# Optimization experiments

Measured on AMD Instinct MI355X. Metric: run time of the kernel, lower is better.

Reference implementation:

```python
import jax, jax.numpy as jnp
import numpy as np

NBITS = 8
NUM_HEADS = 6


def _quant(x, alpha, nbits=NBITS):
    # LSQ-style fake quantization with straight-through estimator.
    qn = -(2 ** (nbits - 1))        # -128
    qp = 2 ** (nbits - 1) - 1       # 127
    s = jnp.clip(x / alpha, qn, qp)
    s = s + jax.lax.stop_gradient(jnp.round(s) - s)  # STE round
    return s * alpha


def setup_inputs() -> dict:
    key = jax.random.key(0)
    ks = jax.random.split(key, 12)
    B, N, C = 2, 2048, 384
    x = jax.random.normal(ks[0], (B, N, C), dtype=jnp.float32)
    w_qkv = jax.random.normal(ks[1], (3 * C, C), dtype=jnp.float32) * 0.02
    w_proj = jax.random.normal(ks[2], (C, C), dtype=jnp.float32) * 0.02
    b_proj = jnp.zeros((C,), dtype=jnp.float32)

    def alpha(k, lo, hi):
        return jax.random.uniform(k, (1,), dtype=jnp.float32, minval=lo, maxval=hi)

    return {
        "x": x,
        "w_qkv": w_qkv,
        "w_proj": w_proj,
        "b_proj": b_proj,
        "a_qkv_w": alpha(ks[3], 0.001, 0.005),
        "a_qkv_a": alpha(ks[4], 0.02, 0.05),
        "a_proj_w": alpha(ks[5], 0.001, 0.005),
        "a_proj_a": alpha(ks[6], 0.02, 0.05),
        "a_q": alpha(ks[7], 0.01, 0.03),
        "a_k": alpha(ks[8], 0.01, 0.03),
        "a_v": alpha(ks[9], 0.01, 0.03),
        "a_attn": alpha(ks[10], 0.01, 0.03),
        "a_attn2": alpha(ks[11], 0.005, 0.01),
    }


def reference(x, w_qkv, w_proj, b_proj, a_qkv_w, a_qkv_a, a_proj_w, a_proj_a,
              a_q, a_k, a_v, a_attn, a_attn2):
    B, N, C = x.shape
    H = NUM_HEADS
    D = C // H
    scale = D ** (-0.5)

    # quantized qkv linear (no bias)
    qkv = _quant(x, a_qkv_a) @ _quant(w_qkv, a_qkv_w).T          # [B,N,3C]
    qkv = qkv.reshape(B, N, 3, H, D).transpose(2, 0, 3, 1, 4)    # [3,B,H,N,D]
    q, k, v = qkv[0], qkv[1], qkv[2]
    q = _quant(q, a_q)
    k = _quant(k, a_k)
    v = _quant(v, a_v)

    attn = jnp.einsum("bhnd,bhmd->bhnm", q, k) * scale           # [B,H,N,N]
    attn = _quant(attn, a_attn)
    attn = jax.nn.softmax(attn, axis=-1)
    attn = _quant(attn, a_attn2)

    out = jnp.einsum("bhnm,bhmd->bhnd", attn, v)                 # [B,H,N,D]
    out = out.transpose(0, 2, 1, 3).reshape(B, N, C)

    # quantized output projection (with bias)
    out = _quant(out, a_proj_a) @ _quant(w_proj, a_proj_w).T + b_proj
    return out
```

## Files before the change

### kernel.cpp

```cpp
#include <hip/hip_runtime.h>
#include <math.h>


typedef int i32x4 __attribute__((ext_vector_type(4)));
typedef float f32x2 __attribute__((ext_vector_type(2)));

#define MFMA_I8(a, b, c) __builtin_amdgcn_mfma_i32_16x16x64_i8(a, b, c, 0, 0, 0)

__device__ __forceinline__ float qclip(float s) {
  return fminf(fmaxf(s, -128.0f), 127.0f);
}

__device__ __forceinline__ float fdivn(float x, float c, float rc) {
  float q0 = x * rc;
  float e = fmaf(-c, q0, x);
  return fmaf(e, rc, q0);
}

__device__ __forceinline__ f32x2 fdivn2(f32x2 x, f32x2 c, f32x2 rc) {
  f32x2 q0 = x * rc;
  f32x2 e = __builtin_elementwise_fma(-c, q0, x);
  return __builtin_elementwise_fma(e, rc, q0);
}

__device__ __forceinline__ void quant16_body(const float* __restrict__ in,
                                             signed char* __restrict__ out,
                                             float a, int i) {
  const float ra = 1.0f / a;
  const float4* p = (const float4*)in + 4 * (size_t)i;
  union { uint4 u; signed char c[16]; } o;
#pragma unroll
  for (int u = 0; u < 4; ++u) {
    float4 v = p[u];
    o.c[4 * u + 0] = (signed char)(int)rintf(qclip(fdivn(v.x, a, ra)));
    o.c[4 * u + 1] = (signed char)(int)rintf(qclip(fdivn(v.y, a, ra)));
    o.c[4 * u + 2] = (signed char)(int)rintf(qclip(fdivn(v.z, a, ra)));
    o.c[4 * u + 3] = (signed char)(int)rintf(qclip(fdivn(v.w, a, ra)));
  }
  *(uint4*)(out + 16 * (size_t)i) = o.u;
}

__global__ __launch_bounds__(256)
void prep(const float* __restrict__ x, const float* __restrict__ wqkv,
          const float* __restrict__ wproj,
          signed char* __restrict__ xq, signed char* __restrict__ wqq,
          signed char* __restrict__ wpq, float* __restrict__ E2,
          const float* __restrict__ a_qkv_a, const float* __restrict__ a_qkv_w,
          const float* __restrict__ a_proj_w, const float* __restrict__ aattn) {
  const int b = blockIdx.x, t = threadIdx.x;
  if (b < 384) {
    int i = b * 256 + t;
    if (i < 98304) quant16_body(x, xq, a_qkv_a[0], i);
  } else if (b < 492) {
    int i = (b - 384) * 256 + t;
    if (i < 27648) quant16_body(wqkv, wqq, a_qkv_w[0], i);
  } else if (b < 528) {
    int i = (b - 492) * 256 + t;
    if (i < 9216) quant16_body(wproj, wpq, a_proj_w[0], i);
  } else {
    int i = (b - 528) * 256 + t;
    float a = aattn[0];
    int vm = (i >> 8) - 128;
    int s = (i & 255) - 128;
    float m = a * (float)vm;
    E2[i] = expf(a * (float)s - m);
  }
}

__global__ __launch_bounds__(256)
void gemm_qkv(const signed char* __restrict__ A, const signed char* __restrict__ W,
              signed char* __restrict__ qws, signed char* __restrict__ kws,
              signed char* __restrict__ vwsT,
              const float* __restrict__ aa, const float* __restrict__ aw,
              const float* __restrict__ aq, const float* __restrict__ ak,
              const float* __restrict__ av) {
  __shared__ int red[2 * 64 * 33];
  const int t = threadIdx.x;
  const int w = t >> 6, lane = t & 63;
  const int lm = lane & 15, quad = lane >> 4;
  const int kw = w >> 1, nw = w & 1;
  const int m0 = blockIdx.x * 64;
  const int n0 = blockIdx.y * 64 + nw * 32;
  i32x4 acc[4][2] = {};
#pragma unroll
  for (int kk = 0; kk < 3; ++kk) {
    int k0 = kw * 192 + kk * 64;
    i32x4 af[4], bf[2];
#pragma unroll
    for (int mt = 0; mt < 4; ++mt)
      af[mt] = *(const i32x4*)(A + (size_t)(m0 + mt * 16 + lm) * 384 + k0 + quad * 16);
#pragma unroll
    for (int nt = 0; nt < 2; ++nt)
      bf[nt] = *(const i32x4*)(W + (size_t)(n0 + nt * 16 + lm) * 384 + k0 + quad * 16);
#pragma unroll
    for (int mt = 0; mt < 4; ++mt)
#pragma unroll
      for (int nt = 0; nt < 2; ++nt)
        acc[mt][nt] = MFMA_I8(af[mt], bf[nt], acc[mt][nt]);
  }
  if (kw == 1) {
    int* rw = red + nw * 2112 + lane * 33;
#pragma unroll
    for (int mt = 0; mt < 4; ++mt)
#pragma unroll
      for (int nt = 0; nt < 2; ++nt)
#pragma unroll
        for (int r = 0; r < 4; ++r)
          rw[mt * 8 + nt * 4 + r] = acc[mt][nt][r];
  }
  __syncthreads();
  if (kw == 0) {
    const int* rw = red + nw * 2112 + lane * 33;
    const float sAB = aa[0] * aw[0];
    const float vaq = aq[0], vak = ak[0], vav = av[0];
    const float rq = 1.0f / vaq, rk = 1.0f / vak, rv = 1.0f / vav;
#pragma unroll
    for (int mt = 0; mt < 4; ++mt) {
#pragma unroll
      for (int nt = 0; nt < 2; ++nt) {
        int cg = n0 + nt * 16 + lm;
        int t3 = cg / 384;
        int rem = cg - t3 * 384;
        int h = rem >> 6, d = rem & 63;
#pragma unroll
        for (int r = 0; r < 4; ++r) {
          int m = m0 + mt * 16 + quad * 4 + r;
          int bb = m >> 11, nn = m & 2047;
          int bh = bb * 6 + h;
          int sum = acc[mt][nt][r] + rw[mt * 8 + nt * 4 + r];
          float val = (float)sum * sAB;
          if (t3 == 0) {
            qws[((size_t)(bh * 2048 + nn) << 6) + d] =
                (signed char)(int)rintf(qclip(fdivn(val, vaq, rq)));
          } else if (t3 == 1) {
            kws[((size_t)(bh * 2048 + nn) << 6) + d] =
                (signed char)(int)rintf(qclip(fdivn(val, vak, rk)));
          } else {
            vwsT[((size_t)((bh << 6) + d) << 11) + nn] =
                (signed char)(int)rintf(qclip(fdivn(val, vav, rv)));
          }
        }
      }
    }
  }
}

#define TROW 2064
__global__ __launch_bounds__(256)
void attn_fused(const signed char* __restrict__ qws, const signed char* __restrict__ kws,
                const signed char* __restrict__ vwsT, const float* __restrict__ E2,
                signed char* __restrict__ ows,
                const float* __restrict__ aq, const float* __restrict__ ak,
                const float* __restrict__ aattn, const float* __restrict__ aattn2,
                const float* __restrict__ av, const float* __restrict__ apa) {
  __shared__ signed char tileS[16 * TROW];
  __shared__ float EfS[4 * 257];
  const int t = threadIdx.x;
  const int w = t >> 6, lane = t & 63;
  const int lm = lane & 15, quad = lane >> 4;
  const int i0 = blockIdx.x * 16;
  const int bh = blockIdx.y;

  const signed char* Qb = qws + ((size_t)bh << 17);
  const signed char* Kb = kws + ((size_t)bh << 17);

  i32x4 bq = *(const i32x4*)(Qb + ((size_t)(i0 + lm) << 6) + quad * 16);
  const float sc = aq[0] * ak[0] * 0.125f;
  const float ia = aattn[0];
  const float ria = 1.0f / ia;
  const f32x2 ia2v = {ia, ia}, ria2v = {ria, ria}, sc2v = {sc, sc};
#pragma unroll 4
  for (int ct = 0; ct < 32; ++ct) {
    int col0 = (w << 9) + ct * 16;
    i32x4 akf = *(const i32x4*)(Kb + ((size_t)(col0 + lm) << 6) + quad * 16);
    i32x4 z = {};
    i32x4 acc = MFMA_I8(akf, bq, z);
    f32x2 sv01 = {(float)acc[0], (float)acc[1]};
    f32x2 sv23 = {(float)acc[2], (float)acc[3]};
    f32x2 q01 = fdivn2(sv01 * sc2v, ia2v, ria2v);
    f32x2 q23 = fdivn2(sv23 * sc2v, ia2v, ria2v);
    union { unsigned int u; signed char c[4]; } pk;
    pk.c[0] = (signed char)(int)rintf(qclip(q01.x));
    pk.c[1] = (signed char)(int)rintf(qclip(q01.y));
    pk.c[2] = (signed char)(int)rintf(qclip(q23.x));
    pk.c[3] = (signed char)(int)rintf(qclip(q23.y));
    *(unsigned int*)(tileS + lm * TROW + col0 + quad * 4) = pk.u;
  }
  __syncthreads();

  const float a2 = aattn2[0];
  const float ra2 = 1.0f / a2;
  const f32x2 a22v = {a2, a2}, ra22v = {ra2, ra2};
  float* Efw = EfS + w * 257;
#pragma unroll
  for (int rr = 0; rr < 4; ++rr) {
    const int row = w * 4 + rr;
    char4* prow = (char4*)(tileS + row * TROW);
    char4 vals[8];
    int vmax = -129;
#pragma unroll
    for (int u = 0; u < 8; ++u) {
      vals[u] = prow[lane + (u << 6)];
      vmax = max(vmax, (int)vals[u].x);
      vmax = max(vmax, (int)vals[u].y);
      vmax = max(vmax, (int)vals[u].z);
      vmax = max(vmax, (int)vals[u].w);
    }
#pragma unroll
    for (int off = 32; off > 0; off >>= 1)
      vmax = max(vmax, __shfl_xor(vmax, off, 64));
#pragma unroll
    for (int u = 0; u < 4; ++u)
      Efw[u * 64 + lane] = E2[((vmax + 128) << 8) + u * 64 + lane];
    const float* Er = Efw + 128;
    float ge[8][4];
    float l = 0.0f;
#pragma unroll
    for (int u = 0; u < 8; ++u) {
      ge[u][0] = Er[(int)vals[u].x];
      ge[u][1] = Er[(int)vals[u].y];
      ge[u][2] = Er[(int)vals[u].z];
      ge[u][3] = Er[(int)vals[u].w];
      l += ge[u][0];
      l += ge[u][1];
      l += ge[u][2];
      l += ge[u][3];
    }
#pragma unroll
    for (int off = 32; off > 0; off >>= 1)
      l += __shfl_xor(l, off, 64);
    const float rl = 1.0f / l;
    const f32x2 l2v = {l, l}, rl2v = {rl, rl};
#pragma unroll
    for (int u = 0; u < 8; ++u) {
      f32x2 g01 = {ge[u][0], ge[u][1]};
      f32x2 g23 = {ge[u][2], ge[u][3]};
      f32x2 t01 = fdivn2(fdivn2(g01, l2v, rl2v), a22v, ra22v);
      f32x2 t23 = fdivn2(fdivn2(g23, l2v, rl2v), a22v, ra22v);
      union { unsigned int ui; signed char c[4]; } pk;
      pk.c[0] = (signed char)(int)rintf(qclip(t01.x));
      pk.c[1] = (signed char)(int)rintf(qclip(t01.y));
      pk.c[2] = (signed char)(int)rintf(qclip(t23.x));
      pk.c[3] = (signed char)(int)rintf(qclip(t23.y));
      *(unsigned int*)(prow + lane + (u << 6)) = pk.ui;
    }
  }
  __syncthreads();

  i32x4 areg[8];
  {
    const signed char* srow = tileS + lm * TROW + (w << 9) + quad * 16;
#pragma unroll
    for (int js = 0; js < 8; ++js)
      areg[js] = *(const i32x4*)(srow + js * 64);
  }
  const signed char* Vb = vwsT + ((size_t)bh << 17) + (w << 9);
  i32x4 acc[4] = {};
#pragma unroll
  for (int js = 0; js < 8; ++js) {
    int j0 = js * 64;
    i32x4 bf[4];
#pragma unroll
    for (int nt = 0; nt < 4; ++nt)
      bf[nt] = *(const i32x4*)(Vb + ((size_t)(nt * 16 + lm) << 11) + j0 + quad * 16);
#pragma unroll
    for (int nt = 0; nt < 4; ++nt)
      acc[nt] = MFMA_I8(areg[js], bf[nt], acc[nt]);
  }

  int* red = (int*)tileS;
  __syncthreads();
  if (w > 0) {
    int* rw = red + (w - 1) * 1088 + lane * 17;
#pragma unroll
    for (int nt = 0; nt < 4; ++nt)
#pragma unroll
      for (int r = 0; r < 4; ++r)
        rw[nt * 4 + r] = acc[nt][r];
  }
  __syncthreads();
  if (w == 0) {
    const float so = a2 * av[0];
    const float ipa = apa[0];
    const float ripa = 1.0f / ipa;
    int bb = bh / 6, h = bh % 6;
#pragma unroll
    for (int nt = 0; nt < 4; ++nt) {
      int d = nt * 16 + lm;
#pragma unroll
      for (int r = 0; r < 4; ++r) {
        int s = acc[nt][r] + red[lane * 17 + nt * 4 + r]
              + red[1088 + lane * 17 + nt * 4 + r]
              + red[2176 + lane * 17 + nt * 4 + r];
        int i = i0 + quad * 4 + r;
        ows[(size_t)((bb << 11) + i) * 384 + (h << 6) + d] =
            (signed char)(int)rintf(qclip(fdivn((float)s * so, ipa, ripa)));
      }
    }
  }
}

__global__ __launch_bounds__(256)
void gemm_proj(const signed char* __restrict__ A, const signed char* __restrict__ W,
               const float* __restrict__ bias, float* __restrict__ out,
               const float* __restrict__ apa, const float* __restrict__ apw) {
  const int t = threadIdx.x;
  const int w = t >> 6, lane = t & 63;
  const int lm = lane & 15, quad = lane >> 4;
  const int wm = w >> 1, wn = w & 1;
  const int m0 = blockIdx.x * 64 + wm * 32;
  const int n0 = blockIdx.y * 64 + wn * 32;
  i32x4 acc[2][2] = {};
  for (int k0 = 0; k0 < 384; k0 += 64) {
    i32x4 af[2], bf[2];
#pragma unroll
    for (int mt = 0; mt < 2; ++mt)
      af[mt] = *(const i32x4*)(A + (size_t)(m0 + mt * 16 + lm) * 384 + k0 + quad * 16);
#pragma unroll
    for (int nt = 0; nt < 2; ++nt)
      bf[nt] = *(const i32x4*)(W + (size_t)(n0 + nt * 16 + lm) * 384 + k0 + quad * 16);
#pragma unroll
    for (int mt = 0; mt < 2; ++mt)
#pragma unroll
      for (int nt = 0; nt < 2; ++nt)
        acc[mt][nt] = MFMA_I8(af[mt], bf[nt], acc[mt][nt]);
  }
  const float sAB = apa[0] * apw[0];
#pragma unroll
  for (int mt = 0; mt < 2; ++mt) {
#pragma unroll
    for (int nt = 0; nt < 2; ++nt) {
      int cg = n0 + nt * 16 + lm;
#pragma unroll
      for (int r = 0; r < 4; ++r) {
        int m = m0 + mt * 16 + quad * 4 + r;
        out[(size_t)m * 384 + cg] = (float)acc[mt][nt][r] * sAB + bias[cg];
      }
    }
  }
}

extern "C" void kernel_launch(void* const* d_in, const int* in_sizes, int n_in,
                              void* d_out, int out_size, void* d_ws, size_t ws_size,
                              hipStream_t stream) {
  const float* x        = (const float*)d_in[0];
  const float* w_qkv    = (const float*)d_in[1];
  const float* w_proj   = (const float*)d_in[2];
  const float* b_proj   = (const float*)d_in[3];
  const float* a_qkv_w  = (const float*)d_in[4];
  const float* a_qkv_a  = (const float*)d_in[5];
  const float* a_proj_w = (const float*)d_in[6];
  const float* a_proj_a = (const float*)d_in[7];
  const float* a_q      = (const float*)d_in[8];
  const float* a_k      = (const float*)d_in[9];
  const float* a_v      = (const float*)d_in[10];
  const float* a_attn   = (const float*)d_in[11];
  const float* a_attn2  = (const float*)d_in[12];

  char* wsb = (char*)d_ws;
  signed char* xq   = (signed char*)(wsb + 0);
  signed char* wqq  = (signed char*)(wsb + 1572864);
  signed char* wpq  = (signed char*)(wsb + 2015232);
  signed char* qws  = (signed char*)(wsb + 2162688);
  signed char* kws  = (signed char*)(wsb + 3735552);
  signed char* vwsT = (signed char*)(wsb + 5308416);
  signed char* ows  = (signed char*)(wsb + 6881280);
  float*       E2   = (float*)(wsb + 8454144);

  prep<<<784, 256, 0, stream>>>(x, w_qkv, w_proj, xq, wqq, wpq, E2,
                                a_qkv_a, a_qkv_w, a_proj_w, a_attn);
  gemm_qkv<<<dim3(64, 18), 256, 0, stream>>>(xq, wqq, qws, kws, vwsT,
                                             a_qkv_a, a_qkv_w, a_q, a_k, a_v);
  attn_fused<<<dim3(128, 12), 256, 0, stream>>>(qws, kws, vwsT, E2, ows,
                                                a_q, a_k, a_attn, a_attn2,
                                                a_v, a_proj_a);
  gemm_proj<<<dim3(64, 6), 256, 0, stream>>>(ows, wpq, b_proj, (float*)d_out,
                                             a_proj_a, a_proj_w);
}
```

Baseline: 153.4 us.

## Batch softmax row loads, use fmed3 clip, split-K proj GEMM, set occupancy hint

The clip helper now uses the hardware med3 instruction instead of a min/max pair. The attention kernel gains a min-waves launch bound, and its softmax stage loads all four rows and their exp-table entries up front so global and LDS latency overlaps across rows. The projection GEMM switches from a 2x2 warp tiling to a split-K layout where warp pairs each cover half of K and reduce through shared memory. The batching raises register pressure, and the split-K path adds an LDS round trip plus a barrier.

```diff
diff --git a/kernel.cpp b/kernel.cpp
--- a/kernel.cpp
+++ b/kernel.cpp
@@ -8,7 +8,7 @@
 #define MFMA_I8(a, b, c) __builtin_amdgcn_mfma_i32_16x16x64_i8(a, b, c, 0, 0, 0)
 
 __device__ __forceinline__ float qclip(float s) {
-  return fminf(fmaxf(s, -128.0f), 127.0f);
+  return __builtin_amdgcn_fmed3f(s, -128.0f, 127.0f);
 }
 
 __device__ __forceinline__ float fdivn(float x, float c, float rc) {
@@ -146,7 +146,7 @@
 }
 
 #define TROW 2064
-__global__ __launch_bounds__(256)
+__global__ __launch_bounds__(256, 4)
 void attn_fused(const signed char* __restrict__ qws, const signed char* __restrict__ kws,
                 const signed char* __restrict__ vwsT, const float* __restrict__ E2,
                 signed char* __restrict__ ows,
@@ -192,35 +192,55 @@
   const float ra2 = 1.0f / a2;
   const f32x2 a22v = {a2, a2}, ra22v = {ra2, ra2};
   float* Efw = EfS + w * 257;
+
+  char4 vals4[4][8];
+#pragma unroll
+  for (int rr = 0; rr < 4; ++rr) {
+    const char4* prow = (const char4*)(tileS + (w * 4 + rr) * TROW);
+#pragma unroll
+    for (int u = 0; u < 8; ++u) vals4[rr][u] = prow[lane + (u << 6)];
+  }
+  int vmax4[4];
+#pragma unroll
+  for (int rr = 0; rr < 4; ++rr) {
+    int vm = -129;
+#pragma unroll
+    for (int u = 0; u < 8; ++u) {
+      vm = max(vm, (int)vals4[rr][u].x);
+      vm = max(vm, (int)vals4[rr][u].y);
+      vm = max(vm, (int)vals4[rr][u].z);
+      vm = max(vm, (int)vals4[rr][u].w);
+    }
+    vmax4[rr] = vm;
+  }
+#pragma unroll
+  for (int off = 32; off > 0; off >>= 1) {
+#pragma unroll
+    for (int rr = 0; rr < 4; ++rr)
+      vmax4[rr] = max(vmax4[rr], __shfl_xor(vmax4[rr], off, 64));
+  }
+  float e2p[4][4];
+#pragma unroll
+  for (int rr = 0; rr < 4; ++rr)
+#pragma unroll
+    for (int u = 0; u < 4; ++u)
+      e2p[rr][u] = E2[((vmax4[rr] + 128) << 8) + u * 64 + lane];
 #pragma unroll
   for (int rr = 0; rr < 4; ++rr) {
     const int row = w * 4 + rr;
     char4* prow = (char4*)(tileS + row * TROW);
-    char4 vals[8];
-    int vmax = -129;
-#pragma unroll
-    for (int u = 0; u < 8; ++u) {
-      vals[u] = prow[lane + (u << 6)];
-      vmax = max(vmax, (int)vals[u].x);
-      vmax = max(vmax, (int)vals[u].y);
-      vmax = max(vmax, (int)vals[u].z);
-      vmax = max(vmax, (int)vals[u].w);
-    }
-#pragma unroll
-    for (int off = 32; off > 0; off >>= 1)
-      vmax = max(vmax, __shfl_xor(vmax, off, 64));
 #pragma unroll
     for (int u = 0; u < 4; ++u)
-      Efw[u * 64 + lane] = E2[((vmax + 128) << 8) + u * 64 + lane];
+      Efw[u * 64 + lane] = e2p[rr][u];
     const float* Er = Efw + 128;
     float ge[8][4];
     float l = 0.0f;
 #pragma unroll
     for (int u = 0; u < 8; ++u) {
-      ge[u][0] = Er[(int)vals[u].x];
-      ge[u][1] = Er[(int)vals[u].y];
-      ge[u][2] = Er[(int)vals[u].z];
-      ge[u][3] = Er[(int)vals[u].w];
+      ge[u][0] = Er[(int)vals4[rr][u].x];
+      ge[u][1] = Er[(int)vals4[rr][u].y];
+      ge[u][2] = Er[(int)vals4[rr][u].z];
+      ge[u][3] = Er[(int)vals4[rr][u].w];
       l += ge[u][0];
       l += ge[u][1];
       l += ge[u][2];
@@ -304,37 +324,55 @@
 void gemm_proj(const signed char* __restrict__ A, const signed char* __restrict__ W,
                const float* __restrict__ bias, float* __restrict__ out,
                const float* __restrict__ apa, const float* __restrict__ apw) {
+  __shared__ int red[2 * 64 * 33];
   const int t = threadIdx.x;
   const int w = t >> 6, lane = t & 63;
   const int lm = lane & 15, quad = lane >> 4;
-  const int wm = w >> 1, wn = w & 1;
-  const int m0 = blockIdx.x * 64 + wm * 32;
-  const int n0 = blockIdx.y * 64 + wn * 32;
-  i32x4 acc[2][2] = {};
-  for (int k0 = 0; k0 < 384; k0 += 64) {
-    i32x4 af[2], bf[2];
-#pragma unroll
-    for (int mt = 0; mt < 2; ++mt)
+  const int kw = w >> 1, nw = w & 1;
+  const int m0 = blockIdx.x * 64;
+  const int n0 = blockIdx.y * 64 + nw * 32;
+  i32x4 acc[4][2] = {};
+#pragma unroll
+  for (int kk = 0; kk < 3; ++kk) {
+    int k0 = kw * 192 + kk * 64;
+    i32x4 af[4], bf[2];
+#pragma unroll
+    for (int mt = 0; mt < 4; ++mt)
       af[mt] = *(const i32x4*)(A + (size_t)(m0 + mt * 16 + lm) * 384 + k0 + quad * 16);
 #pragma unroll
     for (int nt = 0; nt < 2; ++nt)
       bf[nt] = *(const i32x4*)(W + (size_t)(n0 + nt * 16 + lm) * 384 + k0 + quad * 16);
 #pragma unroll
-    for (int mt = 0; mt < 2; ++mt)
+    for (int mt = 0; mt < 4; ++mt)
 #pragma unroll
       for (int nt = 0; nt < 2; ++nt)
         acc[mt][nt] = MFMA_I8(af[mt], bf[nt], acc[mt][nt]);
   }
-  const float sAB = apa[0] * apw[0];
-#pragma unroll
-  for (int mt = 0; mt < 2; ++mt) {
-#pragma unroll
-    for (int nt = 0; nt < 2; ++nt) {
-      int cg = n0 + nt * 16 + lm;
-#pragma unroll
-      for (int r = 0; r < 4; ++r) {
-        int m = m0 + mt * 16 + quad * 4 + r;
-        out[(size_t)m * 384 + cg] = (float)acc[mt][nt][r] * sAB + bias[cg];
+  if (kw == 1) {
+    int* rw = red + nw * 2112 + lane * 33;
+#pragma unroll
+    for (int mt = 0; mt < 4; ++mt)
+#pragma unroll
+      for (int nt = 0; nt < 2; ++nt)
+#pragma unroll
+        for (int r = 0; r < 4; ++r)
+          rw[mt * 8 + nt * 4 + r] = acc[mt][nt][r];
+  }
+  __syncthreads();
+  if (kw == 0) {
+    const int* rw = red + nw * 2112 + lane * 33;
+    const float sAB = apa[0] * apw[0];
+#pragma unroll
+    for (int mt = 0; mt < 4; ++mt) {
+#pragma unroll
+      for (int nt = 0; nt < 2; ++nt) {
+        int cg = n0 + nt * 16 + lm;
+#pragma unroll
+        for (int r = 0; r < 4; ++r) {
+          int m = m0 + mt * 16 + quad * 4 + r;
+          int sum = acc[mt][nt][r] + rw[mt * 8 + nt * 4 + r];
+          out[(size_t)m * 384 + cg] = (float)sum * sAB + bias[cg];
+        }
       }
     }
   }
```

After: 157.6 us. +2.8%, slower.
